# Performance work log

Hardware: AMD Instinct MI355X
Metric: run time of the kernel (lower is better)

The kernel has to match this reference:

```python
import jax, jax.numpy as jnp
import numpy as np

E = 768       # embed dim
NH = 12       # heads
HD = 64       # head dim
WIN = 14      # window size
DEPTH = 12
PATCH = 16
WINDOW_IDX = (0, 1, 3, 4, 6, 7, 9, 10)
EPS = 1e-6


def layer_norm(x, w, b):
    mu = jnp.mean(x, axis=-1, keepdims=True)
    var = jnp.mean(jnp.square(x - mu), axis=-1, keepdims=True)
    return (x - mu) * jax.lax.rsqrt(var + EPS) * w + b


def get_rel_pos(size, rel_pos):
    # q_size == k_size -> direct lookup, no interpolation
    coords = jnp.arange(size)
    rel = coords[:, None] - coords[None, :] + (size - 1)
    return rel_pos[rel]  # (size, size, HD)


def attention(x, qkv_w, qkv_b, proj_w, proj_b, rel_h, rel_w):
    B, H, W, _ = x.shape
    N = H * W
    qkv = (x.reshape(B, N, E) @ qkv_w + qkv_b).reshape(B, N, 3, NH, HD)
    q = qkv[:, :, 0].transpose(0, 2, 1, 3).reshape(B * NH, N, HD)
    k = qkv[:, :, 1].transpose(0, 2, 1, 3).reshape(B * NH, N, HD)
    v = qkv[:, :, 2].transpose(0, 2, 1, 3).reshape(B * NH, N, HD)
    attn = (q * (HD ** -0.5)) @ k.transpose(0, 2, 1)  # (B*NH, N, N)
    # decomposed relative position bias
    Rh = get_rel_pos(H, rel_h)  # (H, H, HD)
    Rw = get_rel_pos(W, rel_w)  # (W, W, HD)
    r_q = q.reshape(B * NH, H, W, HD)
    rh = jnp.einsum('bhwc,hkc->bhwk', r_q, Rh)
    rw = jnp.einsum('bhwc,wkc->bhwk', r_q, Rw)
    attn = attn.reshape(B * NH, H, W, H, W) + rh[:, :, :, :, None] + rw[:, :, :, None, :]
    attn = jax.nn.softmax(attn.reshape(B * NH, N, N), axis=-1)
    out = (attn @ v).reshape(B, NH, H, W, HD).transpose(0, 2, 3, 1, 4).reshape(B, H, W, E)
    return out @ proj_w + proj_b


def window_partition(x, ws):
    B, H, W, C = x.shape
    pad_h, pad_w = (-H) % ws, (-W) % ws
    x = jnp.pad(x, ((0, 0), (0, pad_h), (0, pad_w), (0, 0)))
    Hp, Wp = H + pad_h, W + pad_w
    x = x.reshape(B, Hp // ws, ws, Wp // ws, ws, C).transpose(0, 1, 3, 2, 4, 5)
    return x.reshape(-1, ws, ws, C), (Hp, Wp)


def window_unpartition(win, ws, pad_hw, hw):
    Hp, Wp = pad_hw
    H, W = hw
    B = win.shape[0] // ((Hp // ws) * (Wp // ws))
    x = win.reshape(B, Hp // ws, Wp // ws, ws, ws, -1).transpose(0, 1, 3, 2, 4, 5)
    return x.reshape(B, Hp, Wp, -1)[:, :H, :W]


def _forward(x, patch_w, patch_b, pos_embed,
             ln1_w, ln1_b, qkv_w, qkv_b, proj_w, proj_b,
             rel_h_win, rel_w_win, rel_h_glob, rel_w_glob,
             ln2_w, ln2_b, fc1_w, fc1_b, fc2_w, fc2_b, out_w, out_b):
    # patch embed: conv 16x16 stride 16
    x = jax.lax.conv_general_dilated(
        x, patch_w, (PATCH, PATCH), 'VALID',
        dimension_numbers=('NCHW', 'OIHW', 'NCHW'))
    x = x.transpose(0, 2, 3, 1) + patch_b  # (B, H, W, C)
    x = x + pos_embed
    win_i, glob_i = 0, 0
    for i in range(DEPTH):
        shortcut = x
        h = layer_norm(x, ln1_w[i], ln1_b[i])
        if i in WINDOW_IDX:
            hw = h.shape[1:3]
            h, pad_hw = window_partition(h, WIN)
            h = attention(h, qkv_w[i], qkv_b[i], proj_w[i], proj_b[i],
                          rel_h_win[win_i], rel_w_win[win_i])
            h = window_unpartition(h, WIN, pad_hw, hw)
            win_i += 1
        else:
            h = attention(h, qkv_w[i], qkv_b[i], proj_w[i], proj_b[i],
                          rel_h_glob[glob_i], rel_w_glob[glob_i])
            glob_i += 1
        x = shortcut + h
        h = layer_norm(x, ln2_w[i], ln2_b[i])
        h = jax.nn.gelu(h @ fc1_w[i] + fc1_b[i], approximate=False) @ fc2_w[i] + fc2_b[i]
        x = x + h
    feat = x.transpose(0, 3, 1, 2)  # (B, C, H, W) == 'last_feat'
    return jnp.einsum('bchw,oc->bohw', feat, out_w) + out_b[None, :, None, None]


def setup_inputs() -> dict:
    key = jax.random.key(0)
    ks = iter(jax.random.split(key, 64))
    def n(shape, s=0.02):
        return jax.random.normal(next(ks), shape, jnp.float32) * s
    B, IMG = 2, 512
    G = IMG // PATCH  # 32
    return {
        'x': jax.random.normal(next(ks), (B, 3, IMG, IMG), jnp.float32),
        'patch_w': n((E, 3, PATCH, PATCH)),
        'patch_b': jnp.zeros((E,), jnp.float32),
        'pos_embed': n((1, G, G, E)),
        'ln1_w': jnp.ones((DEPTH, E), jnp.float32),
        'ln1_b': jnp.zeros((DEPTH, E), jnp.float32),
        'qkv_w': n((DEPTH, E, 3 * E)),
        'qkv_b': jnp.zeros((DEPTH, 3 * E), jnp.float32),
        'proj_w': n((DEPTH, E, E)),
        'proj_b': jnp.zeros((DEPTH, E), jnp.float32),
        'rel_h_win': n((8, 2 * WIN - 1, HD)),
        'rel_w_win': n((8, 2 * WIN - 1, HD)),
        'rel_h_glob': n((4, 2 * G - 1, HD)),
        'rel_w_glob': n((4, 2 * G - 1, HD)),
        'ln2_w': jnp.ones((DEPTH, E), jnp.float32),
        'ln2_b': jnp.zeros((DEPTH, E), jnp.float32),
        'fc1_w': n((DEPTH, E, 4 * E)),
        'fc1_b': jnp.zeros((DEPTH, 4 * E), jnp.float32),
        'fc2_w': n((DEPTH, 4 * E, E)),
        'fc2_b': jnp.zeros((DEPTH, E), jnp.float32),
        'out_w': n((256, E)),
        'out_b': jnp.zeros((256,), jnp.float32),
    }


def reference(x, patch_w, patch_b, pos_embed,
              ln1_w, ln1_b, qkv_w, qkv_b, proj_w, proj_b,
              rel_h_win, rel_w_win, rel_h_glob, rel_w_glob,
              ln2_w, ln2_b, fc1_w, fc1_b, fc2_w, fc2_b, out_w, out_b):
    return _forward(x, patch_w, patch_b, pos_embed,
                    ln1_w, ln1_b, qkv_w, qkv_b, proj_w, proj_b,
                    rel_h_win, rel_w_win, rel_h_glob, rel_w_glob,
                    ln2_w, ln2_b, fc1_w, fc1_b, fc2_w, fc2_b, out_w, out_b)
```

## Files before the change

kernel.cpp:

```cpp
#include <hip/hip_runtime.h>
#include <hip/hip_bf16.h>
#include <math.h>

static constexpr int E   = 768;
static constexpr int NH  = 12;
static constexpr int HD  = 64;
static constexpr int Bsz = 2;
static constexpr int G   = 32;
static constexpr int NTOK = G * G;
static constexpr int ROWS = Bsz * NTOK;
static constexpr int WS  = 14;
static constexpr int NWIN_SIDE = 3;
static constexpr int NWIN = NWIN_SIDE * NWIN_SIDE;
static constexpr int BW  = Bsz * NWIN;
static constexpr int NW  = WS * WS;
static constexpr int WROWS = BW * NW;
static constexpr int WIN_MASK = 0x6DB;

typedef __attribute__((ext_vector_type(8))) short short8;
typedef __attribute__((ext_vector_type(4))) float f32x4;
typedef unsigned short ushort_t;

__device__ __forceinline__ unsigned short f2bf(float x) {
  union { float f; unsigned u; } v; v.f = x;
  unsigned r = v.u + 0x7fffu + ((v.u >> 16) & 1u);
  return (unsigned short)(r >> 16);
}
__device__ __forceinline__ float bf2f(unsigned short h) {
  union { unsigned u; float f; } v; v.u = ((unsigned)h) << 16;
  return v.f;
}

__device__ __forceinline__ void glds16(const void* g, void* l) {
  __builtin_amdgcn_global_load_lds(
      (const __attribute__((address_space(1))) unsigned*)g,
      (__attribute__((address_space(3))) unsigned*)l, 16, 0, 0);
}

__global__ __launch_bounds__(256) void ln_kernel(
    const float* __restrict__ in, const float* __restrict__ w,
    const float* __restrict__ b, ushort_t* __restrict__ out) {
  const int wave = threadIdx.x >> 6, lane = threadIdx.x & 63;
  const int row = blockIdx.x * 4 + wave;
  const float4* r4 = (const float4*)(in + (size_t)row * E);
  float4 v[3];
  v[0] = r4[lane]; v[1] = r4[lane + 64]; v[2] = r4[lane + 128];
  float s = 0.f, s2 = 0.f;
#pragma unroll
  for (int i = 0; i < 3; i++) {
    s += v[i].x + v[i].y + v[i].z + v[i].w;
    s2 += v[i].x * v[i].x + v[i].y * v[i].y + v[i].z * v[i].z + v[i].w * v[i].w;
  }
#pragma unroll
  for (int off = 1; off <= 32; off <<= 1) {
    s += __shfl_xor(s, off);
    s2 += __shfl_xor(s2, off);
  }
  const float mean = s * (1.f / E);
  const float var  = s2 * (1.f / E) - mean * mean;
  const float rs   = rsqrtf(var + 1e-6f);
  ushort_t* o = out + (size_t)row * E;
#pragma unroll
  for (int i = 0; i < 3; i++) {
    const int e0 = (lane + i * 64) * 4;
    ushort4 p;
    p.x = f2bf((v[i].x - mean) * rs * w[e0]     + b[e0]);
    p.y = f2bf((v[i].y - mean) * rs * w[e0 + 1] + b[e0 + 1]);
    p.z = f2bf((v[i].z - mean) * rs * w[e0 + 2] + b[e0 + 2]);
    p.w = f2bf((v[i].w - mean) * rs * w[e0 + 3] + b[e0 + 3]);
    *(ushort4*)&o[e0] = p;
  }
}

enum { OP_QKV = 0, OP_GELU = 1, OP_ADD = 2, OP_POS = 3, OP_HEAD = 4 };

template <int OP, int MAP>
__global__ __launch_bounds__(256) void gemm_bt(
    const ushort_t* __restrict__ A, const ushort_t* __restrict__ Bt,
    const float* __restrict__ bias, const float* __restrict__ res,
    const float* __restrict__ pos, void* __restrict__ Cp,
    int M, int N, int K, int ncol) {
  __shared__ ushort_t As[2][64 * 64];
  __shared__ ushort_t Bs[2][64 * 64];
  const int tid = threadIdx.x, wave = tid >> 6, lane = tid & 63;
  const int lx = lane & 15, ly = lane >> 4;

  const int nwg = gridDim.x;
  const int q = nwg >> 3, r = nwg & 7;
  const int xcd = blockIdx.x & 7, loc = blockIdx.x >> 3;
  const int wgid = ((xcd < r) ? xcd * (q + 1) : r * (q + 1) + (xcd - r) * q) + loc;
  const int brow = wgid / ncol, bcol = wgid - brow * ncol;
  const int row0 = brow * 64, col0 = bcol * 64;
  const int wm = (wave >> 1) * 32, wn = (wave & 1) * 32;
  const int rin = lane >> 3, pseg = lane & 7;
  const int lseg = pseg ^ rin;
  f32x4 acc[2][2] = {};

  const ushort_t* aptr[2];
  const ushort_t* bptr[2];
#pragma unroll
  for (int j = 0; j < 2; j++) {
    const int slot = wave * 2 + j;
    int ar = row0 + slot * 8 + rin;
    if (ar >= M) ar = M - 1;
    if (MAP == 2) {
      const int bI = ar >> 10, t = ar & 1023, y = t >> 5, x = t & 31;
      const int by = y / WS, wy = y - by * WS;
      const int bx = x / WS, wx = x - bx * WS;
      const int win = bI * NWIN + by * NWIN_SIDE + bx;
      aptr[j] = &A[((size_t)win * NW + wy * WS + wx) * E + lseg * 8];
    } else {
      aptr[j] = &A[(size_t)ar * K + lseg * 8];
    }
    const int br = col0 + slot * 8 + rin;
    bptr[j] = &Bt[(size_t)br * K + lseg * 8];
  }

#pragma unroll
  for (int j = 0; j < 2; j++) {
    const int slot = wave * 2 + j;
    glds16(aptr[j], &As[0][slot * 512]);
    glds16(bptr[j], &Bs[0][slot * 512]);
  }
  __syncthreads();

  const int nt = K >> 6;
  int cur = 0;
  for (int t = 0; t < nt; t++) {
    if (t + 1 < nt) {
      const int k1 = (t + 1) << 6;
#pragma unroll
      for (int j = 0; j < 2; j++) {
        const int slot = wave * 2 + j;
        glds16(aptr[j] + k1, &As[cur ^ 1][slot * 512]);
        glds16(bptr[j] + k1, &Bs[cur ^ 1][slot * 512]);
      }
    }
#pragma unroll
    for (int kb = 0; kb < 2; kb++) {
      short8 af[2], bfm[2];
#pragma unroll
      for (int m = 0; m < 2; m++) {
        const int rr = wm + m * 16 + lx;
        af[m] = *(const short8*)&As[cur][rr * 64 + (((kb * 4 + ly) ^ (rr & 7)) * 8)];
      }
#pragma unroll
      for (int n = 0; n < 2; n++) {
        const int rr = wn + n * 16 + lx;
        bfm[n] = *(const short8*)&Bs[cur][rr * 64 + (((kb * 4 + ly) ^ (rr & 7)) * 8)];
      }
      __builtin_amdgcn_s_setprio(1);
#pragma unroll
      for (int m = 0; m < 2; m++)
#pragma unroll
        for (int n = 0; n < 2; n++)
          acc[m][n] = __builtin_amdgcn_mfma_f32_16x16x32_bf16(af[m], bfm[n], acc[m][n], 0, 0, 0);
      __builtin_amdgcn_s_setprio(0);
    }
    __syncthreads();
    cur ^= 1;
  }

#pragma unroll
  for (int m = 0; m < 2; m++) {
#pragma unroll
    for (int r4 = 0; r4 < 4; r4++) {
      const int gr = row0 + wm + m * 16 + ly * 4 + r4;
      if (gr >= M) continue;
#pragma unroll
      for (int n = 0; n < 2; n++) {
        const int gc = col0 + wn + n * 16 + lx;
        float v = acc[m][n][r4] + bias[gc];
        if (OP == OP_GELU) v = 0.5f * v * (1.f + erff(v * 0.70710678118654752f));
        if (OP == OP_ADD)  v += res[(size_t)gr * N + gc];
        if (OP == OP_POS)  v += pos[(size_t)(gr & 1023) * N + gc];
        if (OP == OP_QKV || OP == OP_GELU)
          ((ushort_t*)Cp)[(size_t)gr * N + gc] = f2bf(v);
        else if (OP == OP_HEAD)
          ((float*)Cp)[(((size_t)(gr >> 10) * 256 + gc) << 10) | (gr & 1023)] = v;
        else
          ((float*)Cp)[(size_t)gr * N + gc] = v;
      }
    }
  }
}

__global__ __launch_bounds__(128) void attn_mfma(
    const ushort_t* __restrict__ qkv, ushort_t* __restrict__ out,
    const float* __restrict__ relh, const float* __restrict__ relw,
    int Hd, int Wd) {
  const int Ntok = Hd * Wd;
  __shared__ ushort_t smem[11392];
  ushort_t* Ks   = smem;
  ushort_t* Vst  = smem + 2048;
  ushort_t* Ps   = smem + 4608;
  ushort_t* Qs   = smem;
  ushort_t* RelS = smem + 2048;
  ushort_t* Th   = smem + 6144;
  ushort_t* Tw   = smem + 8256;
  ushort_t* khw  = smem + 10368;

  const int tid = threadIdx.x, wave = tid >> 6, lane = tid & 63;
  const int lx = lane & 15, ly = lane >> 4;
  const int bh = blockIdx.y, b = bh / NH, nh = bh % NH;
  const int q0 = blockIdx.x * 32;
  const size_t base = (size_t)b * Ntok * 2304 + nh * 64;

#pragma unroll
  for (int i = 0; i < 2; i++) {
    const int fv = i * 128 + tid;
    const int row = fv >> 3, dv8 = (fv & 7) * 8;
    const int qq = min(q0 + row, Ntok - 1);
    short8 v = *(const short8*)&qkv[base + (size_t)qq * 2304 + dv8];
    *(short8*)&Qs[(row * 64 + dv8) ^ ((row & 7) << 3)] = v;
  }
  for (int k = tid; k < 1024; k += 128) {
    const int kc = min(k, Ntok - 1);
    const int kh = kc / Wd;
    khw[k] = (ushort_t)((kh << 8) | (kc - kh * Wd));
  }
  __syncthreads();

  short8 qa[2];
  {
    const int row = wave * 16 + lx;
#pragma unroll
    for (int kb = 0; kb < 2; kb++)
      qa[kb] = *(const short8*)&Qs[(row * 64 + kb * 32 + ly * 8) ^ ((row & 7) << 3)];
  }
  int qh_r[4], qw_r[4];
#pragma unroll
  for (int r = 0; r < 4; r++) {
    const int qc = min(q0 + wave * 16 + ly * 4 + r, Ntok - 1);
    qh_r[r] = qc / Wd;
    qw_r[r] = qc - qh_r[r] * Wd;
  }

  for (int t = 0; t < 2; t++) {
    const float* rel = t ? relw : relh;
    const int TR = t ? (2 * Wd - 1) : (2 * Hd - 1);
    __syncthreads();
#pragma unroll
    for (int i = 0; i < 4; i++) {
      const int fv = i * 128 + tid;
      const int row = fv >> 3, c8 = (fv & 7) * 8;
      short8 v = {};
      if (row < TR) {
        const float* rp = &rel[(size_t)row * 64 + c8];
        const float4 a = *(const float4*)rp;
        const float4 bq = *(const float4*)(rp + 4);
        v[0] = (short)f2bf(a.x);  v[1] = (short)f2bf(a.y);
        v[2] = (short)f2bf(a.z);  v[3] = (short)f2bf(a.w);
        v[4] = (short)f2bf(bq.x); v[5] = (short)f2bf(bq.y);
        v[6] = (short)f2bf(bq.z); v[7] = (short)f2bf(bq.w);
      }
      *(short8*)&RelS[(row * 64 + c8) ^ ((row & 7) << 3)] = v;
    }
    __syncthreads();
    const int NT = (TR + 15) >> 4;
    ushort_t* T = t ? Tw : Th;
    for (int nt = 0; nt < NT; nt++) {
      f32x4 a = {};
      __builtin_amdgcn_s_setprio(1);
#pragma unroll
      for (int kb = 0; kb < 2; kb++) {
        const int rrow = nt * 16 + lx;
        short8 bfv = *(const short8*)&RelS[(rrow * 64 + kb * 32 + ly * 8) ^ ((rrow & 7) << 3)];
        a = __builtin_amdgcn_mfma_f32_16x16x32_bf16(qa[kb], bfv, a, 0, 0, 0);
      }
      __builtin_amdgcn_s_setprio(0);
#pragma unroll
      for (int reg = 0; reg < 4; reg++)
        T[(wave * 16 + ly * 4 + reg) * 66 + nt * 16 + lx] = f2bf(a[reg]);
    }
  }

  f32x4 o[4] = {};
  float m_[4], l_[4];
#pragma unroll
  for (int r = 0; r < 4; r++) { m_[r] = -3e38f; l_[r] = 0.f; }

  const int nkt = (Ntok + 31) >> 5;
  const int srow = tid >> 3, c7 = tid & 7, dv8s = c7 * 8;
  const int vswz = (c7 & 3) << 3;

  short8 kpre[2], vpre[2];
#pragma unroll
  for (int i = 0; i < 2; i++) {
    const int gk = srow + i * 16;
    short8 kv = {}, vv = {};
    if (gk < Ntok) {
      kv = *(const short8*)&qkv[base + 768 + (size_t)gk * 2304 + dv8s];
      vv = *(const short8*)&qkv[base + 1536 + (size_t)gk * 2304 + dv8s];
    }
    kpre[i] = kv; vpre[i] = vv;
  }

  for (int kt = 0; kt < nkt; kt++) {
    __syncthreads();
#pragma unroll
    for (int i = 0; i < 2; i++) {
      const int row = srow + i * 16;
      *(short8*)&Ks[(row * 64 + dv8s) ^ ((row & 7) << 3)] = kpre[i];
      const int kcol = row ^ vswz;
#pragma unroll
      for (int j = 0; j < 8; j++)
        Vst[(dv8s + j) * 40 + kcol] = (ushort_t)vpre[i][j];
    }
    if (kt + 1 < nkt) {
#pragma unroll
      for (int i = 0; i < 2; i++) {
        const int gk = (kt + 1) * 32 + srow + i * 16;
        short8 kv = {}, vv = {};
        if (gk < Ntok) {
          kv = *(const short8*)&qkv[base + 768 + (size_t)gk * 2304 + dv8s];
          vv = *(const short8*)&qkv[base + 1536 + (size_t)gk * 2304 + dv8s];
        }
        kpre[i] = kv; vpre[i] = vv;
      }
    }
    __syncthreads();

    f32x4 c[2] = {};
    __builtin_amdgcn_s_setprio(1);
#pragma unroll
    for (int kb = 0; kb < 2; kb++)
#pragma unroll
      for (int ct = 0; ct < 2; ct++) {
        const int krow = ct * 16 + lx;
        short8 kf = *(const short8*)&Ks[(krow * 64 + kb * 32 + ly * 8) ^ ((krow & 7) << 3)];
        c[ct] = __builtin_amdgcn_mfma_f32_16x16x32_bf16(qa[kb], kf, c[ct], 0, 0, 0);
      }
    __builtin_amdgcn_s_setprio(0);

    const int k0a = kt * 32 + lx, k1a = k0a + 16;
    const int tv0 = khw[k0a], tv1 = khw[k1a];
    const int kh0 = tv0 >> 8, kw0 = tv0 & 255;
    const int kh1 = tv1 >> 8, kw1 = tv1 & 255;
    float pv0[4], pv1[4], mt[4];
#pragma unroll
    for (int r = 0; r < 4; r++) {
      const int trow = (wave * 16 + ly * 4 + r) * 66;
      float s0 = c[0][r] * 0.125f + bf2f(Th[trow + qh_r[r] - kh0 + Hd - 1])
               + bf2f(Tw[trow + qw_r[r] - kw0 + Wd - 1]);
      float s1 = c[1][r] * 0.125f + bf2f(Th[trow + qh_r[r] - kh1 + Hd - 1])
               + bf2f(Tw[trow + qw_r[r] - kw1 + Wd - 1]);
      if (k0a >= Ntok) s0 = -1e30f;
      if (k1a >= Ntok) s1 = -1e30f;
      pv0[r] = s0; pv1[r] = s1;
      mt[r] = fmaxf(s0, s1);
    }
    const float dmax = fmaxf(fmaxf(mt[0] - m_[0], mt[1] - m_[1]),
                             fmaxf(mt[2] - m_[2], mt[3] - m_[3]));
    if (!__all(dmax <= 8.f)) {
#pragma unroll
      for (int r = 0; r < 4; r++) {
        float mr = mt[r];
#pragma unroll
        for (int off = 1; off <= 8; off <<= 1) mr = fmaxf(mr, __shfl_xor(mr, off));
        const float mn = fmaxf(m_[r], mr);
        const float sc = __expf(m_[r] - mn);
        m_[r] = mn; l_[r] *= sc;
#pragma unroll
        for (int dt = 0; dt < 4; dt++) o[dt][r] *= sc;
      }
    }
#pragma unroll
    for (int r = 0; r < 4; r++) {
      const float p0 = __expf(pv0[r] - m_[r]);
      const float p1 = __expf(pv1[r] - m_[r]);
      l_[r] += p0 + p1;
      const int pb = wave * 640 + (ly * 4 + r) * 40;
      Ps[pb + lx]      = f2bf(p0);
      Ps[pb + 16 + lx] = f2bf(p1);
    }
    short8 pf = *(const short8*)&Ps[wave * 640 + lx * 40 + ly * 8];
    __builtin_amdgcn_s_setprio(1);
#pragma unroll
    for (int dt = 0; dt < 4; dt++) {
      const int drow = dt * 16 + lx;
      short8 vf = *(const short8*)&Vst[drow * 40 + ((ly * 8) ^ (((drow >> 3) & 3) << 3))];
      o[dt] = __builtin_amdgcn_mfma_f32_16x16x32_bf16(pf, vf, o[dt], 0, 0, 0);
    }
    __builtin_amdgcn_s_setprio(0);
  }

#pragma unroll
  for (int r = 0; r < 4; r++) {
#pragma unroll
    for (int off = 1; off <= 8; off <<= 1) l_[r] += __shfl_xor(l_[r], off);
    const int qq = q0 + wave * 16 + ly * 4 + r;
    if (qq >= Ntok) continue;
    const float inv = 1.f / l_[r];
#pragma unroll
    for (int dt = 0; dt < 4; dt++)
      out[((size_t)b * Ntok + qq) * E + nh * 64 + dt * 16 + lx] = f2bf(o[dt][r] * inv);
  }
}

__global__ __launch_bounds__(128) void qkv_winpart(
    const ushort_t* __restrict__ qi, const float* __restrict__ qkvb,
    ushort_t* __restrict__ qw) {
  const int row = blockIdx.x;
  const int win = row / NW, t = row - win * NW;
  const int wy = t / WS, wx = t - wy * WS;
  const int b = win / NWIN, wr = win - b * NWIN;
  const int by = wr / NWIN_SIDE, bx = wr - by * NWIN_SIDE;
  const int y = by * WS + wy, x = bx * WS + wx;
  short8* dst = (short8*)(qw + (size_t)row * 2304);
  if (y < G && x < G) {
    const short8* src = (const short8*)(qi + (((size_t)b * G + y) * G + x) * 2304);
    for (int e = threadIdx.x; e < 288; e += 128) dst[e] = src[e];
  } else {
    for (int e = threadIdx.x; e < 288; e += 128) {
      short8 v;
#pragma unroll
      for (int j = 0; j < 8; j++) v[j] = (short)f2bf(qkvb[e * 8 + j]);
      dst[e] = v;
    }
  }
}

__global__ __launch_bounds__(256) void im2col(const float* __restrict__ x,
                                              ushort_t* __restrict__ out) {
  const int blk = blockIdx.x;
  const int b = blk >> 10, t = blk & 1023, gy = t >> 5, gx = t & 31;
  for (int k = threadIdx.x; k < 768; k += 256) {
    const int ci = k >> 8, rem = k & 255, py = rem >> 4, px = rem & 15;
    out[(size_t)blk * 768 + k] =
        f2bf(x[(((size_t)b * 3 + ci) * 512 + gy * 16 + py) * 512 + gx * 16 + px]);
  }
}

__global__ __launch_bounds__(256) void prep_wt64(
    const float* __restrict__ qkvw, const float* __restrict__ projw,
    const float* __restrict__ fc1w, const float* __restrict__ fc2w,
    ushort_t* __restrict__ wq, ushort_t* __restrict__ wp,
    ushort_t* __restrict__ w1, ushort_t* __restrict__ w2) {
  __shared__ float tile[64][65];
  const int blk = blockIdx.x;
  const float* W; ushort_t* Wt; int Kd, Nd, tn, tk;
  if (blk < 432)       { W = qkvw;  Wt = wq; Kd = 768;  Nd = 2304; tn = blk % 36;          tk = blk / 36; }
  else if (blk < 576)  { W = projw; Wt = wp; Kd = 768;  Nd = 768;  tn = (blk - 432) % 12;  tk = (blk - 432) / 12; }
  else if (blk < 1152) { W = fc1w;  Wt = w1; Kd = 768;  Nd = 3072; tn = (blk - 576) % 48;  tk = (blk - 576) / 48; }
  else                 { W = fc2w;  Wt = w2; Kd = 3072; Nd = 768;  tn = (blk - 1152) % 12; tk = (blk - 1152) / 12; }
  const int k0 = tk * 64, n0 = tn * 64;
  const int kr = threadIdx.x >> 2, cg = (threadIdx.x & 3) * 16;
  const float* src = &W[(size_t)(k0 + kr) * Nd + n0 + cg];
#pragma unroll
  for (int j = 0; j < 4; j++) {
    const float4 v = *(const float4*)&src[j * 4];
    tile[kr][cg + j * 4 + 0] = v.x;
    tile[kr][cg + j * 4 + 1] = v.y;
    tile[kr][cg + j * 4 + 2] = v.z;
    tile[kr][cg + j * 4 + 3] = v.w;
  }
  __syncthreads();
  const int nr = kr;
  short8 o0, o1;
#pragma unroll
  for (int j = 0; j < 8; j++) o0[j] = (short)f2bf(tile[cg + j][nr]);
#pragma unroll
  for (int j = 0; j < 8; j++) o1[j] = (short)f2bf(tile[cg + 8 + j][nr]);
  ushort_t* dst = &Wt[(size_t)(n0 + nr) * Kd + k0 + cg];
  *(short8*)&dst[0] = o0;
  *(short8*)&dst[8] = o1;
}

__global__ __launch_bounds__(256) void cast_bf16(const float* __restrict__ in,
                                                 ushort_t* __restrict__ out, int n) {
  const int idx = (blockIdx.x * 256 + threadIdx.x) * 4;
  if (idx + 3 < n) {
    const float4 v = *(const float4*)&in[idx];
    ushort4 p;
    p.x = f2bf(v.x); p.y = f2bf(v.y); p.z = f2bf(v.z); p.w = f2bf(v.w);
    *(ushort4*)&out[idx] = p;
  }
}

extern "C" void kernel_launch(void* const* d_in, const int* in_sizes, int n_in,
                              void* d_out, int out_size, void* d_ws, size_t ws_size,
                              hipStream_t stream) {
  const float* x_in     = (const float*)d_in[0];
  const float* patch_w  = (const float*)d_in[1];
  const float* patch_b  = (const float*)d_in[2];
  const float* pos_emb  = (const float*)d_in[3];
  const float* ln1_w    = (const float*)d_in[4];
  const float* ln1_b    = (const float*)d_in[5];
  const float* qkv_w    = (const float*)d_in[6];
  const float* qkv_b    = (const float*)d_in[7];
  const float* proj_w   = (const float*)d_in[8];
  const float* proj_b   = (const float*)d_in[9];
  const float* rel_h_w  = (const float*)d_in[10];
  const float* rel_w_w  = (const float*)d_in[11];
  const float* rel_h_g  = (const float*)d_in[12];
  const float* rel_w_g  = (const float*)d_in[13];
  const float* ln2_w    = (const float*)d_in[14];
  const float* ln2_b    = (const float*)d_in[15];
  const float* fc1_w    = (const float*)d_in[16];
  const float* fc1_b    = (const float*)d_in[17];
  const float* fc2_w    = (const float*)d_in[18];
  const float* fc2_b    = (const float*)d_in[19];
  const float* out_w    = (const float*)d_in[20];
  const float* out_b    = (const float*)d_in[21];
  float* outp = (float*)d_out;

  float* xbuf = (float*)d_ws;
  ushort_t* hb16    = (ushort_t*)(xbuf + (size_t)ROWS * E);
  ushort_t* qkvimg  = hb16 + (size_t)ROWS * E;
  ushort_t* qkvwin  = qkvimg + (size_t)ROWS * 3 * E;
  ushort_t* attnw16 = qkvwin + (size_t)WROWS * 3 * E;
  ushort_t* h1b16   = attnw16 + (size_t)WROWS * E;
  ushort_t* wq      = h1b16 + (size_t)ROWS * 4 * E;
  ushort_t* wp      = wq + (size_t)2304 * 768;
  ushort_t* w1      = wp + (size_t)768 * 768;
  ushort_t* w2      = w1 + (size_t)3072 * 768;
  ushort_t* pwT16   = w2 + (size_t)768 * 3072;
  ushort_t* headW16 = pwT16 + (size_t)768 * 768;
  ushort_t* imb16 = hb16;

  cast_bf16<<<576, 256, 0, stream>>>(patch_w, pwT16, 768 * 768);
  cast_bf16<<<192, 256, 0, stream>>>(out_w, headW16, 256 * 768);

  im2col<<<ROWS, 256, 0, stream>>>(x_in, imb16);
  gemm_bt<OP_POS, 0><<<12 * 32, 256, 0, stream>>>(
      imb16, pwT16, patch_b, nullptr, pos_emb, xbuf, ROWS, E, E, 12);

  int win_i = 0, glob_i = 0;
  for (int i = 0; i < 12; i++) {
    const bool is_win = (WIN_MASK >> i) & 1;

    prep_wt64<<<1728, 256, 0, stream>>>(
        qkv_w + (size_t)i * E * 3 * E, proj_w + (size_t)i * E * E,
        fc1_w + (size_t)i * E * 4 * E, fc2_w + (size_t)i * 4 * E * E,
        wq, wp, w1, w2);

    ln_kernel<<<ROWS / 4, 256, 0, stream>>>(xbuf, ln1_w + i * E, ln1_b + i * E, hb16);

    gemm_bt<OP_QKV, 0><<<36 * 32, 256, 0, stream>>>(
        hb16, wq, qkv_b + i * 3 * E, nullptr, nullptr, qkvimg, ROWS, 3 * E, E, 36);

    if (is_win) {
      qkv_winpart<<<WROWS, 128, 0, stream>>>(qkvimg, qkv_b + i * 3 * E, qkvwin);
      attn_mfma<<<dim3(7, BW * NH), 128, 0, stream>>>(
          qkvwin, attnw16, rel_h_w + (size_t)win_i * (2 * WS - 1) * HD,
          rel_w_w + (size_t)win_i * (2 * WS - 1) * HD, WS, WS);
      win_i++;
      gemm_bt<OP_ADD, 2><<<12 * 32, 256, 0, stream>>>(
          attnw16, wp, proj_b + i * E, xbuf, nullptr, xbuf, ROWS, E, E, 12);
    } else {
      attn_mfma<<<dim3(32, Bsz * NH), 128, 0, stream>>>(
          qkvimg, attnw16, rel_h_g + (size_t)glob_i * (2 * G - 1) * HD,
          rel_w_g + (size_t)glob_i * (2 * G - 1) * HD, G, G);
      glob_i++;
      gemm_bt<OP_ADD, 0><<<12 * 32, 256, 0, stream>>>(
          attnw16, wp, proj_b + i * E, xbuf, nullptr, xbuf, ROWS, E, E, 12);
    }

    ln_kernel<<<ROWS / 4, 256, 0, stream>>>(xbuf, ln2_w + i * E, ln2_b + i * E, hb16);
    gemm_bt<OP_GELU, 0><<<48 * 32, 256, 0, stream>>>(
        hb16, w1, fc1_b + i * 4 * E, nullptr, nullptr, h1b16, ROWS, 4 * E, E, 48);
    gemm_bt<OP_ADD, 0><<<12 * 32, 256, 0, stream>>>(
        h1b16, w2, fc2_b + i * E, xbuf, nullptr, xbuf, ROWS, E, 4 * E, 12);
  }

  cast_bf16<<<1536, 256, 0, stream>>>(xbuf, hb16, ROWS * E);
  gemm_bt<OP_HEAD, 0><<<4 * 32, 256, 0, stream>>>(
      hb16, headW16, out_b, nullptr, nullptr, outp, ROWS, 256, E, 4);
}
```

Baseline: 1.842 ms.

## Compute each 64x64 GEMM tile with a single wave and drop block barriers

The bf16 GEMM kernel moves from four waves, each owning a 32x32 quadrant, to one wave computing the whole 64x64 tile with a 4x4 grid of MFMA accumulators. `__syncthreads` is replaced by explicit `s_waitcnt vmcnt` waits on the async global-to-LDS loads, with a sched barrier. The aim is to cut barrier overhead and improve fragment reuse per wave. In exchange each workgroup has only 64 threads and LDS limits how many fit per CU, so far fewer waves are resident to hide memory latency. The `vmcnt(32)` threshold also looks too loose to guarantee the current tile has landed before it is read.

```diff
diff --git a/kernel.cpp b/kernel.cpp
--- a/kernel.cpp
+++ b/kernel.cpp
@@ -75,14 +75,14 @@
 enum { OP_QKV = 0, OP_GELU = 1, OP_ADD = 2, OP_POS = 3, OP_HEAD = 4 };
 
 template <int OP, int MAP>
-__global__ __launch_bounds__(256) void gemm_bt(
+__global__ __launch_bounds__(64) void gemm_w(
     const ushort_t* __restrict__ A, const ushort_t* __restrict__ Bt,
     const float* __restrict__ bias, const float* __restrict__ res,
     const float* __restrict__ pos, void* __restrict__ Cp,
     int M, int N, int K, int ncol) {
   __shared__ ushort_t As[2][64 * 64];
   __shared__ ushort_t Bs[2][64 * 64];
-  const int tid = threadIdx.x, wave = tid >> 6, lane = tid & 63;
+  const int lane = threadIdx.x;
   const int lx = lane & 15, ly = lane >> 4;
 
   const int nwg = gridDim.x;
@@ -91,17 +91,15 @@
   const int wgid = ((xcd < r) ? xcd * (q + 1) : r * (q + 1) + (xcd - r) * q) + loc;
   const int brow = wgid / ncol, bcol = wgid - brow * ncol;
   const int row0 = brow * 64, col0 = bcol * 64;
-  const int wm = (wave >> 1) * 32, wn = (wave & 1) * 32;
   const int rin = lane >> 3, pseg = lane & 7;
   const int lseg = pseg ^ rin;
-  f32x4 acc[2][2] = {};
-
-  const ushort_t* aptr[2];
-  const ushort_t* bptr[2];
-#pragma unroll
-  for (int j = 0; j < 2; j++) {
-    const int slot = wave * 2 + j;
-    int ar = row0 + slot * 8 + rin;
+  f32x4 acc[4][4] = {};
+
+  const ushort_t* aptr[8];
+  const ushort_t* bptr[8];
+#pragma unroll
+  for (int j = 0; j < 8; j++) {
+    int ar = row0 + j * 8 + rin;
     if (ar >= M) ar = M - 1;
     if (MAP == 2) {
       const int bI = ar >> 10, t = ar & 1023, y = t >> 5, x = t & 31;
@@ -112,64 +110,60 @@
     } else {
       aptr[j] = &A[(size_t)ar * K + lseg * 8];
     }
-    const int br = col0 + slot * 8 + rin;
+    const int br = col0 + j * 8 + rin;
     bptr[j] = &Bt[(size_t)br * K + lseg * 8];
   }
 
 #pragma unroll
-  for (int j = 0; j < 2; j++) {
-    const int slot = wave * 2 + j;
-    glds16(aptr[j], &As[0][slot * 512]);
-    glds16(bptr[j], &Bs[0][slot * 512]);
-  }
-  __syncthreads();
+  for (int j = 0; j < 8; j++) {
+    glds16(aptr[j], &As[0][j * 512]);
+    glds16(bptr[j], &Bs[0][j * 512]);
+  }
 
   const int nt = K >> 6;
-  int cur = 0;
   for (int t = 0; t < nt; t++) {
+    const int cur = t & 1;
     if (t + 1 < nt) {
       const int k1 = (t + 1) << 6;
 #pragma unroll
-      for (int j = 0; j < 2; j++) {
-        const int slot = wave * 2 + j;
-        glds16(aptr[j] + k1, &As[cur ^ 1][slot * 512]);
-        glds16(bptr[j] + k1, &Bs[cur ^ 1][slot * 512]);
-      }
-    }
+      for (int j = 0; j < 8; j++) {
+        glds16(aptr[j] + k1, &As[cur ^ 1][j * 512]);
+        glds16(bptr[j] + k1, &Bs[cur ^ 1][j * 512]);
+      }
+      asm volatile("s_waitcnt vmcnt(32)" ::: "memory");
+    } else {
+      asm volatile("s_waitcnt vmcnt(0)" ::: "memory");
+    }
+    __builtin_amdgcn_sched_barrier(0);
 #pragma unroll
     for (int kb = 0; kb < 2; kb++) {
-      short8 af[2], bfm[2];
-#pragma unroll
-      for (int m = 0; m < 2; m++) {
-        const int rr = wm + m * 16 + lx;
-        af[m] = *(const short8*)&As[cur][rr * 64 + (((kb * 4 + ly) ^ (rr & 7)) * 8)];
-      }
-#pragma unroll
-      for (int n = 0; n < 2; n++) {
-        const int rr = wn + n * 16 + lx;
-        bfm[n] = *(const short8*)&Bs[cur][rr * 64 + (((kb * 4 + ly) ^ (rr & 7)) * 8)];
+      short8 af[4], bfm[4];
+#pragma unroll
+      for (int m = 0; m < 4; m++) {
+        const int rr = m * 16 + lx;
+        const int co = (((kb * 4 + ly) ^ (rr & 7)) * 8);
+        af[m]  = *(const short8*)&As[cur][rr * 64 + co];
+        bfm[m] = *(const short8*)&Bs[cur][rr * 64 + co];
       }
       __builtin_amdgcn_s_setprio(1);
 #pragma unroll
-      for (int m = 0; m < 2; m++)
-#pragma unroll
-        for (int n = 0; n < 2; n++)
+      for (int m = 0; m < 4; m++)
+#pragma unroll
+        for (int n = 0; n < 4; n++)
           acc[m][n] = __builtin_amdgcn_mfma_f32_16x16x32_bf16(af[m], bfm[n], acc[m][n], 0, 0, 0);
       __builtin_amdgcn_s_setprio(0);
     }
-    __syncthreads();
-    cur ^= 1;
-  }
-
-#pragma unroll
-  for (int m = 0; m < 2; m++) {
+  }
+
+#pragma unroll
+  for (int m = 0; m < 4; m++) {
 #pragma unroll
     for (int r4 = 0; r4 < 4; r4++) {
-      const int gr = row0 + wm + m * 16 + ly * 4 + r4;
+      const int gr = row0 + m * 16 + ly * 4 + r4;
       if (gr >= M) continue;
 #pragma unroll
-      for (int n = 0; n < 2; n++) {
-        const int gc = col0 + wn + n * 16 + lx;
+      for (int n = 0; n < 4; n++) {
+        const int gc = col0 + n * 16 + lx;
         float v = acc[m][n][r4] + bias[gc];
         if (OP == OP_GELU) v = 0.5f * v * (1.f + erff(v * 0.70710678118654752f));
         if (OP == OP_ADD)  v += res[(size_t)gr * N + gc];
@@ -523,7 +517,7 @@
   cast_bf16<<<192, 256, 0, stream>>>(out_w, headW16, 256 * 768);
 
   im2col<<<ROWS, 256, 0, stream>>>(x_in, imb16);
-  gemm_bt<OP_POS, 0><<<12 * 32, 256, 0, stream>>>(
+  gemm_w<OP_POS, 0><<<12 * 32, 64, 0, stream>>>(
       imb16, pwT16, patch_b, nullptr, pos_emb, xbuf, ROWS, E, E, 12);
 
   int win_i = 0, glob_i = 0;
@@ -537,7 +531,7 @@
 
     ln_kernel<<<ROWS / 4, 256, 0, stream>>>(xbuf, ln1_w + i * E, ln1_b + i * E, hb16);
 
-    gemm_bt<OP_QKV, 0><<<36 * 32, 256, 0, stream>>>(
+    gemm_w<OP_QKV, 0><<<36 * 32, 64, 0, stream>>>(
         hb16, wq, qkv_b + i * 3 * E, nullptr, nullptr, qkvimg, ROWS, 3 * E, E, 36);
 
     if (is_win) {
@@ -546,25 +540,25 @@
           qkvwin, attnw16, rel_h_w + (size_t)win_i * (2 * WS - 1) * HD,
           rel_w_w + (size_t)win_i * (2 * WS - 1) * HD, WS, WS);
       win_i++;
-      gemm_bt<OP_ADD, 2><<<12 * 32, 256, 0, stream>>>(
+      gemm_w<OP_ADD, 2><<<12 * 32, 64, 0, stream>>>(
           attnw16, wp, proj_b + i * E, xbuf, nullptr, xbuf, ROWS, E, E, 12);
     } else {
       attn_mfma<<<dim3(32, Bsz * NH), 128, 0, stream>>>(
           qkvimg, attnw16, rel_h_g + (size_t)glob_i * (2 * G - 1) * HD,
           rel_w_g + (size_t)glob_i * (2 * G - 1) * HD, G, G);
       glob_i++;
-      gemm_bt<OP_ADD, 0><<<12 * 32, 256, 0, stream>>>(
+      gemm_w<OP_ADD, 0><<<12 * 32, 64, 0, stream>>>(
           attnw16, wp, proj_b + i * E, xbuf, nullptr, xbuf, ROWS, E, E, 12);
     }
 
     ln_kernel<<<ROWS / 4, 256, 0, stream>>>(xbuf, ln2_w + i * E, ln2_b + i * E, hb16);
-    gemm_bt<OP_GELU, 0><<<48 * 32, 256, 0, stream>>>(
+    gemm_w<OP_GELU, 0><<<48 * 32, 64, 0, stream>>>(
         hb16, w1, fc1_b + i * 4 * E, nullptr, nullptr, h1b16, ROWS, 4 * E, E, 48);
-    gemm_bt<OP_ADD, 0><<<12 * 32, 256, 0, stream>>>(
+    gemm_w<OP_ADD, 0><<<12 * 32, 64, 0, stream>>>(
         h1b16, w2, fc2_b + i * E, xbuf, nullptr, xbuf, ROWS, E, 4 * E, 12);
   }
 
   cast_bf16<<<1536, 256, 0, stream>>>(xbuf, hb16, ROWS * E);
-  gemm_bt<OP_HEAD, 0><<<4 * 32, 256, 0, stream>>>(
+  gemm_w<OP_HEAD, 0><<<4 * 32, 64, 0, stream>>>(
       hb16, headW16, out_b, nullptr, nullptr, outp, ROWS, 256, E, 4);
 }
```

After: 2.611 ms. 41.8% more time.
